# Optimization experiments

Hardware: AMD Instinct MI355X
Metric: run time of the kernel (lower is better)

Reference implementation:

```python
import jax, jax.numpy as jnp
import numpy as np

PAD = 1
K = 3  # kernel_size


def conv2d(x, w, b):
    y = jax.lax.conv_general_dilated(
        x, w, window_strides=(1, 1), padding=((PAD, PAD), (PAD, PAD)),
        dimension_numbers=("NCHW", "OIHW", "NCHW"))
    return y + b[None, :, None, None]


def deform_conv2d(x, offset, weight, bias):
    # torchvision.ops.deform_conv2d semantics (stride=1, dilation=1, 1 offset group)
    B, C, H, W = x.shape
    O = weight.shape[0]
    K2 = K * K
    off = offset.reshape(B, K2, 2, H, W)  # [...,0]=dy, [...,1]=dx
    ky, kx = jnp.meshgrid(jnp.arange(K), jnp.arange(K), indexing="ij")
    ky = ky.reshape(K2).astype(x.dtype)
    kx = kx.reshape(K2).astype(x.dtype)
    hh = jnp.arange(H, dtype=x.dtype)
    ww = jnp.arange(W, dtype=x.dtype)
    # sampling coords, shape [B, K2, H, W]
    py = off[:, :, 0] + ky[None, :, None, None] + hh[None, None, :, None] - PAD
    px = off[:, :, 1] + kx[None, :, None, None] + ww[None, None, None, :] - PAD

    y0 = jnp.floor(py)
    x0 = jnp.floor(px)
    wy = (py - y0)[:, None]  # [B,1,K2,H,W]
    wx = (px - x0)[:, None]

    xf = x.reshape(B, C, H * W)

    def gather(iy, ix):
        valid = (iy >= 0) & (iy < H) & (ix >= 0) & (ix < W)
        iyc = jnp.clip(iy, 0, H - 1).astype(jnp.int32)
        ixc = jnp.clip(ix, 0, W - 1).astype(jnp.int32)
        idx = (iyc * W + ixc).reshape(B, 1, K2 * H * W)
        v = jnp.take_along_axis(xf, idx, axis=2).reshape(B, C, K2, H, W)
        return v * valid.reshape(B, 1, K2, H, W).astype(x.dtype)

    v00 = gather(y0, x0)
    v01 = gather(y0, x0 + 1)
    v10 = gather(y0 + 1, x0)
    v11 = gather(y0 + 1, x0 + 1)
    sampled = (v00 * (1 - wy) * (1 - wx) + v01 * (1 - wy) * wx
               + v10 * wy * (1 - wx) + v11 * wy * wx)  # [B,C,K2,H,W]
    out = jnp.einsum("bckhw,ock->bohw", sampled, weight.reshape(O, C, K2))
    return out + bias[None, :, None, None]


def setup_inputs() -> dict:
    key = jax.random.key(0)
    k1, k2, k3, k4, k5 = jax.random.split(key, 5)
    B, C, H, W = 4, 64, 192, 192
    O = 64
    x = jax.random.normal(k1, (B, C, H, W), dtype=jnp.float32)
    w_off = jax.random.normal(k2, (2 * K * K, C, K, K), dtype=jnp.float32) * 0.05
    b_off = jnp.zeros((2 * K * K,), dtype=jnp.float32)
    w_conv = jax.random.normal(k3, (O, C, K, K), dtype=jnp.float32) * (1.0 / np.sqrt(C * K * K))
    b_conv = jax.random.normal(k4, (O,), dtype=jnp.float32) * 0.01
    return {"x": x, "w_off": w_off, "b_off": b_off, "w_conv": w_conv, "b_conv": b_conv}


def reference(x, w_off, b_off, w_conv, b_conv):
    offset = conv2d(x, w_off, b_off)
    y = deform_conv2d(x, offset, w_conv, b_conv)
    return conv2d(y, w_conv, b_conv)  # module reuses self.conv on deform output
```

## Files before the change

kernel.cpp:

```cpp
#include <hip/hip_runtime.h>

constexpr int B = 4;
constexpr int C = 64;
constexpr int O = 64;
constexpr int OOFF = 18;
constexpr int H = 192;
constexpr int W = 192;

typedef __attribute__((ext_vector_type(8))) short short8;
typedef __attribute__((ext_vector_type(4))) float float4v;

__device__ inline ushort f2bf(float f) {
  unsigned u = __float_as_uint(f);
  unsigned r = (u + 0x7fffu + ((u >> 16) & 1u)) >> 16;
  return (ushort)r;
}

__global__ __launch_bounds__(256) void k_prep_wB(const float* __restrict__ w_conv,
                                                 ushort* __restrict__ wBf) {
  const int i = blockIdx.x * 256 + threadIdx.x;
  if (i >= 9 * 2 * 4 * 64 * 8) return;
  const int j = i & 7;
  const int lane = (i >> 3) & 63;
  const int nt = (i >> 9) & 3;
  const int kstep = (i >> 11) & 1;
  const int kk = i >> 12;
  const int n = nt + 4 * (lane & 15);
  const int c = kstep * 32 + ((lane >> 4) & 3) * 8 + j;
  wBf[i] = f2bf(w_conv[((size_t)n * C + c) * 9 + kk]);
}

__global__ __launch_bounds__(256) void k_prep_wOff(const float* __restrict__ w_off,
                                                   ushort* __restrict__ wOf) {
  const int i = blockIdx.x * 256 + threadIdx.x;
  if (i >= 9 * 2 * 2 * 64 * 8) return;
  const int j = i & 7;
  const int lane = (i >> 3) & 63;
  const int nt = (i >> 9) & 1;
  const int ks = (i >> 10) & 1;
  const int kk = i >> 11;
  const int n = nt * 16 + (lane & 15);
  const int c = ks * 32 + ((lane >> 4) & 3) * 8 + j;
  wOf[i] = (n < OOFF) ? f2bf(w_off[((size_t)n * C + c) * 9 + kk]) : (ushort)0;
}

__global__ __launch_bounds__(256) void k_transpose_bf(const float* __restrict__ x,
                                                      ushort* __restrict__ xtb) {
  __shared__ float tile[64][17];
  const int w0 = blockIdx.x * 16;
  const int h = blockIdx.y;
  const int b = blockIdx.z;
  const int tid = threadIdx.x;

  const int wl = tid & 15;
  const int c0 = tid >> 4;
#pragma unroll
  for (int r = 0; r < 4; ++r) {
    const int c = c0 + r * 16;
    tile[c][wl] = x[(((size_t)b * C + c) * H + h) * W + w0 + wl];
  }
  __syncthreads();
  const int c = tid & 63;
  const int qq = tid >> 6;
#pragma unroll
  for (int r = 0; r < 4; ++r) {
    const int wq = qq + r * 4;
    xtb[(((size_t)b * H + h) * W + w0 + wq) * C + c] = f2bf(tile[c][wq]);
  }
}

__global__ __launch_bounds__(256) void k_conv_off_mfma(
    const ushort* __restrict__ xtb, const ushort* __restrict__ wOf,
    const float* __restrict__ b_off, float* __restrict__ offp) {
  const int w0 = blockIdx.x * 16;
  const int b = blockIdx.z;
  const int tid = threadIdx.x;
  const int wave = tid >> 6, lane = tid & 63;
  const int col = lane & 15, quad = lane >> 4;
  const int h0 = blockIdx.y * 8 + wave * 2;

  float4v acc[2][2];
#pragma unroll
  for (int mt = 0; mt < 2; ++mt)
#pragma unroll
    for (int nt = 0; nt < 2; ++nt) acc[mt][nt] = (float4v){0.f, 0.f, 0.f, 0.f};

#pragma unroll 1
  for (int kk = 0; kk < 9; ++kk) {
    const int ky = kk / 3, kx = kk % 3;
    const int ww = w0 + col + kx - 1;
    const bool wok = (unsigned)ww < (unsigned)W;
    const int wwc = min(max(ww, 0), W - 1);

    short8 bfr[2][2];
#pragma unroll
    for (int ks = 0; ks < 2; ++ks)
#pragma unroll
      for (int nt = 0; nt < 2; ++nt)
        bfr[ks][nt] = *(const short8*)&wOf[((((size_t)kk * 2 + ks) * 2 + nt) * 64 + lane) * 8];

    short8 afr[2][2];
#pragma unroll
    for (int mt = 0; mt < 2; ++mt) {
      const int hh = h0 + mt + ky - 1;
      const bool ok = wok && ((unsigned)hh < (unsigned)H);
      const int hhc = min(max(hh, 0), H - 1);
      const ushort* pa = xtb + (((size_t)b * H + hhc) * W + wwc) * C + quad * 8;
#pragma unroll
      for (int ks = 0; ks < 2; ++ks) {
        short8 v = (short8)0;
        if (ok) v = *(const short8*)(pa + ks * 32);
        afr[mt][ks] = v;
      }
    }
#pragma unroll
    for (int ks = 0; ks < 2; ++ks)
#pragma unroll
      for (int mt = 0; mt < 2; ++mt)
#pragma unroll
        for (int nt = 0; nt < 2; ++nt)
          acc[mt][nt] = __builtin_amdgcn_mfma_f32_16x16x32_bf16(afr[mt][ks], bfr[ks][nt],
                                                                acc[mt][nt], 0, 0, 0);
  }

#pragma unroll
  for (int mt = 0; mt < 2; ++mt) {
    const int h = h0 + mt;
#pragma unroll
    for (int nt = 0; nt < 2; ++nt) {
      const int o = nt * 16 + col;
      if (o < OOFF) {
        const float bias = b_off[o];
#pragma unroll
        for (int r = 0; r < 4; ++r) {
          const int w = w0 + quad * 4 + r;
          offp[(((size_t)b * H + h) * W + w) * OOFF + o] = acc[mt][nt][r] + bias;
        }
      }
    }
  }
}

__global__ __launch_bounds__(256, 3) void k_deform_mfma(
    const ushort* __restrict__ xtb, const float* __restrict__ offp,
    const ushort* __restrict__ wBf, const float* __restrict__ b_conv,
    ushort* __restrict__ yt) {
  __shared__ ushort sA[2][2][4][64][8];

  const int bid = blockIdx.x;
  const int xcd = bid & 7;
  const int s = bid >> 3;
  const int b = xcd >> 1;
  const int half = xcd & 1;
  const int th = half * 12 + s / 24;
  const int tw = s % 24;
  const int h0 = th * 8, w0 = tw * 8;

  const int tid = threadIdx.x;
  const int wave = tid >> 6, lane = tid & 63;
  const int p = tid >> 2, qtr = tid & 3;
  const int prow = p >> 3, pcol = p & 7;
  const int h = h0 + prow, w = w0 + pcol;
  const int ks_w = qtr >> 1;
  const int q2 = (qtr & 1) * 2;

  const float* po = offp + ((size_t)(b * H + h) * W + w) * OOFF;
  float2 offv[9];
#pragma unroll
  for (int kk = 0; kk < 9; ++kk) offv[kk] = *(const float2*)(po + 2 * kk);

  const ushort* xb = xtb + (size_t)b * H * W * C + qtr * 16;

  uint4 G[2][8];
  float4 aw[2];

  auto issue = [&](int kk, int buf) {
    const float dy = offv[kk].x, dx = offv[kk].y;
    const int ky = kk / 3, kx = kk % 3;
    const float pyf = dy + (float)(ky + h - 1);
    const float pxf = dx + (float)(kx + w - 1);
    const float fy0 = floorf(pyf), fx0 = floorf(pxf);
    const float wy = pyf - fy0, wx = pxf - fx0;
    const int iy0 = (int)fy0, ix0 = (int)fx0;
    const int iy1 = iy0 + 1, ix1 = ix0 + 1;
    const bool vy0 = (unsigned)iy0 < (unsigned)H;
    const bool vy1 = (unsigned)iy1 < (unsigned)H;
    const bool vx0 = (unsigned)ix0 < (unsigned)W;
    const bool vx1 = (unsigned)ix1 < (unsigned)W;
    aw[buf].x = (vy0 && vx0) ? (1.f - wy) * (1.f - wx) : 0.f;
    aw[buf].y = (vy0 && vx1) ? (1.f - wy) * wx : 0.f;
    aw[buf].z = (vy1 && vx0) ? wy * (1.f - wx) : 0.f;
    aw[buf].w = (vy1 && vx1) ? wy * wx : 0.f;
    const int cy0 = min(max(iy0, 0), H - 1), cy1 = min(max(iy1, 0), H - 1);
    const int cx0 = min(max(ix0, 0), W - 1), cx1 = min(max(ix1, 0), W - 1);
    const uint4* p00 = (const uint4*)(xb + ((size_t)cy0 * W + cx0) * C);
    const uint4* p01 = (const uint4*)(xb + ((size_t)cy0 * W + cx1) * C);
    const uint4* p10 = (const uint4*)(xb + ((size_t)cy1 * W + cx0) * C);
    const uint4* p11 = (const uint4*)(xb + ((size_t)cy1 * W + cx1) * C);
    G[buf][0] = p00[0]; G[buf][1] = p00[1];
    G[buf][2] = p01[0]; G[buf][3] = p01[1];
    G[buf][4] = p10[0]; G[buf][5] = p10[1];
    G[buf][6] = p11[0]; G[buf][7] = p11[1];
  };

  float4v acc[4];
#pragma unroll
  for (int nt = 0; nt < 4; ++nt) acc[nt] = (float4v){0.f, 0.f, 0.f, 0.f};

  issue(0, 0);
#pragma unroll
  for (int kk = 0; kk < 9; ++kk) {
    const int buf = kk & 1;
    if (kk < 8) issue(kk + 1, buf ^ 1);

    const float a00 = aw[buf].x, a01 = aw[buf].y;
    const float a10 = aw[buf].z, a11 = aw[buf].w;
    uint pk[8];
#pragma unroll
    for (int i = 0; i < 8; ++i) {
      const uint u00 = ((const uint*)&G[buf][0])[i];
      const uint u01 = ((const uint*)&G[buf][2])[i];
      const uint u10 = ((const uint*)&G[buf][4])[i];
      const uint u11 = ((const uint*)&G[buf][6])[i];
      const float lo = __uint_as_float(u00 << 16) * a00 + __uint_as_float(u01 << 16) * a01 +
                       __uint_as_float(u10 << 16) * a10 + __uint_as_float(u11 << 16) * a11;
      const float hi = __uint_as_float(u00 & 0xffff0000u) * a00 +
                       __uint_as_float(u01 & 0xffff0000u) * a01 +
                       __uint_as_float(u10 & 0xffff0000u) * a10 +
                       __uint_as_float(u11 & 0xffff0000u) * a11;
      pk[i] = (uint)f2bf(lo) | ((uint)f2bf(hi) << 16);
    }
    *(uint4*)&sA[buf][ks_w][p >> 4][(p & 15) | (q2 << 4)][0] = *(const uint4*)&pk[0];
    *(uint4*)&sA[buf][ks_w][p >> 4][(p & 15) | ((q2 + 1) << 4)][0] = *(const uint4*)&pk[4];
    __syncthreads();

#pragma unroll
    for (int ks = 0; ks < 2; ++ks) {
      const short8 a = *(const short8*)&sA[buf][ks][wave][lane][0];
#pragma unroll
      for (int nt = 0; nt < 4; ++nt) {
        const short8 bb = *(const short8*)&wBf[((((size_t)kk * 2 + ks) * 4 + nt) * 64 + lane) * 8];
        acc[nt] = __builtin_amdgcn_mfma_f32_16x16x32_bf16(a, bb, acc[nt], 0, 0, 0);
      }
    }
  }

  const int quad = lane >> 4, c16 = lane & 15;
  float bias[4];
#pragma unroll
  for (int nt = 0; nt < 4; ++nt) bias[nt] = b_conv[4 * c16 + nt];
#pragma unroll
  for (int r = 0; r < 4; ++r) {
    const int pp = wave * 16 + quad * 4 + r;
    const int hrow = h0 + (pp >> 3), wcol = w0 + (pp & 7);
    uint2 u;
    u.x = (uint)f2bf(acc[0][r] + bias[0]) | ((uint)f2bf(acc[1][r] + bias[1]) << 16);
    u.y = (uint)f2bf(acc[2][r] + bias[2]) | ((uint)f2bf(acc[3][r] + bias[3]) << 16);
    *(uint2*)&yt[((size_t)(b * H + hrow) * W + wcol) * C + 4 * c16] = u;
  }
}

__global__ __launch_bounds__(256) void k_conv_main_mfma(
    const ushort* __restrict__ yt, const ushort* __restrict__ wBf,
    const float* __restrict__ b_conv, float* __restrict__ out) {
  const int w0 = blockIdx.x * 16;
  const int b = blockIdx.z;
  const int tid = threadIdx.x;
  const int wave = tid >> 6, lane = tid & 63;
  const int col = lane & 15, quad = lane >> 4;
  const int h0 = blockIdx.y * 8 + wave * 2;

  float4v acc[2][4];
#pragma unroll
  for (int mt = 0; mt < 2; ++mt)
#pragma unroll
    for (int nt = 0; nt < 4; ++nt) acc[mt][nt] = (float4v){0.f, 0.f, 0.f, 0.f};

#pragma unroll 1
  for (int kk = 0; kk < 9; ++kk) {
    const int ky = kk / 3, kx = kk % 3;
    const int ww = w0 + col + kx - 1;
    const bool wok = (unsigned)ww < (unsigned)W;
    const int wwc = min(max(ww, 0), W - 1);

    short8 bfr[2][4];
#pragma unroll
    for (int ks = 0; ks < 2; ++ks)
#pragma unroll
      for (int nt = 0; nt < 4; ++nt)
        bfr[ks][nt] = *(const short8*)&wBf[((((size_t)kk * 2 + ks) * 4 + nt) * 64 + lane) * 8];

    short8 afr[2][2];
#pragma unroll
    for (int mt = 0; mt < 2; ++mt) {
      const int hh = h0 + mt + ky - 1;
      const bool ok = wok && ((unsigned)hh < (unsigned)H);
      const int hhc = min(max(hh, 0), H - 1);
      const ushort* pa = yt + (((size_t)b * H + hhc) * W + wwc) * C + quad * 8;
#pragma unroll
      for (int ks = 0; ks < 2; ++ks) {
        short8 v = (short8)0;
        if (ok) v = *(const short8*)(pa + ks * 32);
        afr[mt][ks] = v;
      }
    }
#pragma unroll
    for (int ks = 0; ks < 2; ++ks)
#pragma unroll
      for (int mt = 0; mt < 2; ++mt)
#pragma unroll
        for (int nt = 0; nt < 4; ++nt)
          acc[mt][nt] = __builtin_amdgcn_mfma_f32_16x16x32_bf16(afr[mt][ks], bfr[ks][nt],
                                                                acc[mt][nt], 0, 0, 0);
  }

  float bias[4];
#pragma unroll
  for (int nt = 0; nt < 4; ++nt) bias[nt] = b_conv[4 * col + nt];
#pragma unroll
  for (int mt = 0; mt < 2; ++mt) {
    const int h = h0 + mt;
#pragma unroll
    for (int nt = 0; nt < 4; ++nt) {
      const int oc = 4 * col + nt;
      float4 v;
      v.x = acc[mt][nt][0] + bias[nt];
      v.y = acc[mt][nt][1] + bias[nt];
      v.z = acc[mt][nt][2] + bias[nt];
      v.w = acc[mt][nt][3] + bias[nt];
      *(float4*)&out[(((size_t)b * O + oc) * H + h) * W + w0 + quad * 4] = v;
    }
  }
}

extern "C" void kernel_launch(void* const* d_in, const int* in_sizes, int n_in,
                              void* d_out, int out_size, void* d_ws, size_t ws_size,
                              hipStream_t stream) {
  const float* x = (const float*)d_in[0];
  const float* w_off = (const float*)d_in[1];
  const float* b_off = (const float*)d_in[2];
  const float* w_conv = (const float*)d_in[3];
  const float* b_conv = (const float*)d_in[4];
  float* out = (float*)d_out;

  float* offp = (float*)d_ws;
  ushort* xtb = (ushort*)(offp + (size_t)B * H * W * OOFF);
  ushort* yt = xtb + (size_t)B * H * W * C;
  ushort* wBf = yt + (size_t)B * H * W * C;
  ushort* wOf = wBf + 36864;

  const dim3 blk(256);
  k_prep_wB<<<dim3(144), blk, 0, stream>>>(w_conv, wBf);
  k_prep_wOff<<<dim3(72), blk, 0, stream>>>(w_off, wOf);
  k_transpose_bf<<<dim3(W / 16, H, B), blk, 0, stream>>>(x, xtb);
  k_conv_off_mfma<<<dim3(W / 16, H / 8, B), blk, 0, stream>>>(xtb, wOf, b_off, offp);
  k_deform_mfma<<<dim3(2304), blk, 0, stream>>>(xtb, offp, wBf, b_conv, yt);
  k_conv_main_mfma<<<dim3(W / 16, H / 8, B), blk, 0, stream>>>(yt, wBf, b_conv, out);
}
```

Before: 224.0 us.

## Merge prep kernels, software-pipeline conv loads, use packed bf16 conversions

Folds the two weight-prep kernels and the x transpose into a single launch, removing two kernel launches. Both MFMA convolution kernels now fully unroll the 9-tap loop and double-buffer the A/B fragment loads so the next tap's global loads overlap the current tap's MFMAs. The deform bilinear blend uses packed 2-wide float math, and bf16 rounding now goes through native __bf16 conversions, which may map to hardware pack instructions. The extra prefetch buffers raise register pressure and may lower occupancy.

```diff
diff --git a/kernel.cpp b/kernel.cpp
--- a/kernel.cpp
+++ b/kernel.cpp
@@ -9,63 +9,74 @@
 
 typedef __attribute__((ext_vector_type(8))) short short8;
 typedef __attribute__((ext_vector_type(4))) float float4v;
+typedef __attribute__((ext_vector_type(2))) float f32x2;
+typedef __attribute__((ext_vector_type(2))) uint u32x2;
+typedef __attribute__((ext_vector_type(2))) __bf16 bf16x2;
 
 __device__ inline ushort f2bf(float f) {
-  unsigned u = __float_as_uint(f);
-  unsigned r = (u + 0x7fffu + ((u >> 16) & 1u)) >> 16;
-  return (ushort)r;
-}
-
-__global__ __launch_bounds__(256) void k_prep_wB(const float* __restrict__ w_conv,
-                                                 ushort* __restrict__ wBf) {
-  const int i = blockIdx.x * 256 + threadIdx.x;
-  if (i >= 9 * 2 * 4 * 64 * 8) return;
-  const int j = i & 7;
-  const int lane = (i >> 3) & 63;
-  const int nt = (i >> 9) & 3;
-  const int kstep = (i >> 11) & 1;
-  const int kk = i >> 12;
-  const int n = nt + 4 * (lane & 15);
-  const int c = kstep * 32 + ((lane >> 4) & 3) * 8 + j;
-  wBf[i] = f2bf(w_conv[((size_t)n * C + c) * 9 + kk]);
-}
-
-__global__ __launch_bounds__(256) void k_prep_wOff(const float* __restrict__ w_off,
-                                                   ushort* __restrict__ wOf) {
-  const int i = blockIdx.x * 256 + threadIdx.x;
-  if (i >= 9 * 2 * 2 * 64 * 8) return;
-  const int j = i & 7;
-  const int lane = (i >> 3) & 63;
-  const int nt = (i >> 9) & 1;
-  const int ks = (i >> 10) & 1;
-  const int kk = i >> 11;
-  const int n = nt * 16 + (lane & 15);
-  const int c = ks * 32 + ((lane >> 4) & 3) * 8 + j;
-  wOf[i] = (n < OOFF) ? f2bf(w_off[((size_t)n * C + c) * 9 + kk]) : (ushort)0;
-}
-
-__global__ __launch_bounds__(256) void k_transpose_bf(const float* __restrict__ x,
-                                                      ushort* __restrict__ xtb) {
+  return __builtin_bit_cast(ushort, (__bf16)f);
+}
+__device__ inline uint pk2bf(float lo, float hi) {
+  bf16x2 v;
+  v.x = (__bf16)lo;
+  v.y = (__bf16)hi;
+  return __builtin_bit_cast(uint, v);
+}
+__device__ inline f32x2 upk(uint u) {
+  u32x2 t;
+  t.x = u << 16;
+  t.y = u & 0xffff0000u;
+  return __builtin_bit_cast(f32x2, t);
+}
+
+__global__ __launch_bounds__(256) void k_pre(const float* __restrict__ x,
+                                             ushort* __restrict__ xtb,
+                                             const float* __restrict__ w_conv,
+                                             ushort* __restrict__ wBf,
+                                             const float* __restrict__ w_off,
+                                             ushort* __restrict__ wOf) {
   __shared__ float tile[64][17];
-  const int w0 = blockIdx.x * 16;
-  const int h = blockIdx.y;
-  const int b = blockIdx.z;
+  const int bid = blockIdx.x;
   const int tid = threadIdx.x;
-
-  const int wl = tid & 15;
-  const int c0 = tid >> 4;
-#pragma unroll
-  for (int r = 0; r < 4; ++r) {
-    const int c = c0 + r * 16;
-    tile[c][wl] = x[(((size_t)b * C + c) * H + h) * W + w0 + wl];
-  }
-  __syncthreads();
-  const int c = tid & 63;
-  const int qq = tid >> 6;
-#pragma unroll
-  for (int r = 0; r < 4; ++r) {
-    const int wq = qq + r * 4;
-    xtb[(((size_t)b * H + h) * W + w0 + wq) * C + c] = f2bf(tile[c][wq]);
+  if (bid < 9216) {
+    const int w0 = (bid % 12) * 16;
+    const int h = (bid / 12) % 192;
+    const int b = bid / 2304;
+    const int wl = tid & 15;
+    const int c0 = tid >> 4;
+#pragma unroll
+    for (int r = 0; r < 4; ++r) {
+      const int c = c0 + r * 16;
+      tile[c][wl] = x[(((size_t)b * C + c) * H + h) * W + w0 + wl];
+    }
+    __syncthreads();
+    const int c = tid & 63;
+    const int qq = tid >> 6;
+#pragma unroll
+    for (int r = 0; r < 4; ++r) {
+      const int wq = qq + r * 4;
+      xtb[(((size_t)b * H + h) * W + w0 + wq) * C + c] = f2bf(tile[c][wq]);
+    }
+  } else if (bid < 9360) {
+    const int i = (bid - 9216) * 256 + tid;
+    const int j = i & 7;
+    const int lane = (i >> 3) & 63;
+    const int nt = (i >> 9) & 3;
+    const int kstep = (i >> 11) & 1;
+    const int kk = i >> 12;
+    const int n = nt + 4 * (lane & 15);
+    const int c = kstep * 32 + ((lane >> 4) & 3) * 8 + j;
+    wBf[i] = f2bf(w_conv[((size_t)n * C + c) * 9 + kk]);
+  } else {
+    const int i = (bid - 9360) * 256 + tid;
+    const int j = i & 7;
+    const int lane = (i >> 3) & 63;
+    const int nt = (i >> 9) & 1;
+    const int ks = (i >> 10) & 1;
+    const int kk = i >> 11;
+    const int n = nt * 16 + (lane & 15);
+    const int c = ks * 32 + ((lane >> 4) & 3) * 8 + j;
+    wOf[i] = (n < OOFF) ? f2bf(w_off[((size_t)n * C + c) * 9 + kk]) : (ushort)0;
   }
 }
 
@@ -85,21 +96,19 @@
 #pragma unroll
     for (int nt = 0; nt < 2; ++nt) acc[mt][nt] = (float4v){0.f, 0.f, 0.f, 0.f};
 
-#pragma unroll 1
-  for (int kk = 0; kk < 9; ++kk) {
+  short8 bfr[2][2][2];
+  short8 afr[2][2][2];
+
+  auto load = [&](int kk, int pb) {
     const int ky = kk / 3, kx = kk % 3;
     const int ww = w0 + col + kx - 1;
     const bool wok = (unsigned)ww < (unsigned)W;
     const int wwc = min(max(ww, 0), W - 1);
-
-    short8 bfr[2][2];
 #pragma unroll
     for (int ks = 0; ks < 2; ++ks)
 #pragma unroll
       for (int nt = 0; nt < 2; ++nt)
-        bfr[ks][nt] = *(const short8*)&wOf[((((size_t)kk * 2 + ks) * 2 + nt) * 64 + lane) * 8];
-
-    short8 afr[2][2];
+        bfr[pb][ks][nt] = *(const short8*)&wOf[((((size_t)kk * 2 + ks) * 2 + nt) * 64 + lane) * 8];
 #pragma unroll
     for (int mt = 0; mt < 2; ++mt) {
       const int hh = h0 + mt + ky - 1;
@@ -110,16 +119,23 @@
       for (int ks = 0; ks < 2; ++ks) {
         short8 v = (short8)0;
         if (ok) v = *(const short8*)(pa + ks * 32);
-        afr[mt][ks] = v;
+        afr[pb][mt][ks] = v;
       }
     }
+  };
+
+  load(0, 0);
+#pragma unroll
+  for (int kk = 0; kk < 9; ++kk) {
+    const int pb = kk & 1;
+    if (kk < 8) load(kk + 1, pb ^ 1);
 #pragma unroll
     for (int ks = 0; ks < 2; ++ks)
 #pragma unroll
       for (int mt = 0; mt < 2; ++mt)
 #pragma unroll
         for (int nt = 0; nt < 2; ++nt)
-          acc[mt][nt] = __builtin_amdgcn_mfma_f32_16x16x32_bf16(afr[mt][ks], bfr[ks][nt],
+          acc[mt][nt] = __builtin_amdgcn_mfma_f32_16x16x32_bf16(afr[pb][mt][ks], bfr[pb][ks][nt],
                                                                 acc[mt][nt], 0, 0, 0);
   }
 
@@ -213,8 +229,10 @@
     const int buf = kk & 1;
     if (kk < 8) issue(kk + 1, buf ^ 1);
 
-    const float a00 = aw[buf].x, a01 = aw[buf].y;
-    const float a10 = aw[buf].z, a11 = aw[buf].w;
+    const f32x2 a00 = {aw[buf].x, aw[buf].x};
+    const f32x2 a01 = {aw[buf].y, aw[buf].y};
+    const f32x2 a10 = {aw[buf].z, aw[buf].z};
+    const f32x2 a11 = {aw[buf].w, aw[buf].w};
     uint pk[8];
 #pragma unroll
     for (int i = 0; i < 8; ++i) {
@@ -222,13 +240,8 @@
       const uint u01 = ((const uint*)&G[buf][2])[i];
       const uint u10 = ((const uint*)&G[buf][4])[i];
       const uint u11 = ((const uint*)&G[buf][6])[i];
-      const float lo = __uint_as_float(u00 << 16) * a00 + __uint_as_float(u01 << 16) * a01 +
-                       __uint_as_float(u10 << 16) * a10 + __uint_as_float(u11 << 16) * a11;
-      const float hi = __uint_as_float(u00 & 0xffff0000u) * a00 +
-                       __uint_as_float(u01 & 0xffff0000u) * a01 +
-                       __uint_as_float(u10 & 0xffff0000u) * a10 +
-                       __uint_as_float(u11 & 0xffff0000u) * a11;
-      pk[i] = (uint)f2bf(lo) | ((uint)f2bf(hi) << 16);
+      f32x2 sv = upk(u00) * a00 + upk(u01) * a01 + upk(u10) * a10 + upk(u11) * a11;
+      pk[i] = pk2bf(sv.x, sv.y);
     }
     *(uint4*)&sA[buf][ks_w][p >> 4][(p & 15) | (q2 << 4)][0] = *(const uint4*)&pk[0];
     *(uint4*)&sA[buf][ks_w][p >> 4][(p & 15) | ((q2 + 1) << 4)][0] = *(const uint4*)&pk[4];
@@ -254,8 +267,8 @@
     const int pp = wave * 16 + quad * 4 + r;
     const int hrow = h0 + (pp >> 3), wcol = w0 + (pp & 7);
     uint2 u;
-    u.x = (uint)f2bf(acc[0][r] + bias[0]) | ((uint)f2bf(acc[1][r] + bias[1]) << 16);
-    u.y = (uint)f2bf(acc[2][r] + bias[2]) | ((uint)f2bf(acc[3][r] + bias[3]) << 16);
+    u.x = pk2bf(acc[0][r] + bias[0], acc[1][r] + bias[1]);
+    u.y = pk2bf(acc[2][r] + bias[2], acc[3][r] + bias[3]);
     *(uint2*)&yt[((size_t)(b * H + hrow) * W + wcol) * C + 4 * c16] = u;
   }
 }
@@ -276,21 +289,19 @@
 #pragma unroll
     for (int nt = 0; nt < 4; ++nt) acc[mt][nt] = (float4v){0.f, 0.f, 0.f, 0.f};
 
-#pragma unroll 1
-  for (int kk = 0; kk < 9; ++kk) {
+  short8 bfr[2][2][4];
+  short8 afr[2][2][2];
+
+  auto load = [&](int kk, int pb) {
     const int ky = kk / 3, kx = kk % 3;
     const int ww = w0 + col + kx - 1;
     const bool wok = (unsigned)ww < (unsigned)W;
     const int wwc = min(max(ww, 0), W - 1);
-
-    short8 bfr[2][4];
 #pragma unroll
     for (int ks = 0; ks < 2; ++ks)
 #pragma unroll
       for (int nt = 0; nt < 4; ++nt)
-        bfr[ks][nt] = *(const short8*)&wBf[((((size_t)kk * 2 + ks) * 4 + nt) * 64 + lane) * 8];
-
-    short8 afr[2][2];
+        bfr[pb][ks][nt] = *(const short8*)&wBf[((((size_t)kk * 2 + ks) * 4 + nt) * 64 + lane) * 8];
 #pragma unroll
     for (int mt = 0; mt < 2; ++mt) {
       const int hh = h0 + mt + ky - 1;
@@ -301,16 +312,23 @@
       for (int ks = 0; ks < 2; ++ks) {
         short8 v = (short8)0;
         if (ok) v = *(const short8*)(pa + ks * 32);
-        afr[mt][ks] = v;
+        afr[pb][mt][ks] = v;
       }
     }
+  };
+
+  load(0, 0);
+#pragma unroll
+  for (int kk = 0; kk < 9; ++kk) {
+    const int pb = kk & 1;
+    if (kk < 8) load(kk + 1, pb ^ 1);
 #pragma unroll
     for (int ks = 0; ks < 2; ++ks)
 #pragma unroll
       for (int mt = 0; mt < 2; ++mt)
 #pragma unroll
         for (int nt = 0; nt < 4; ++nt)
-          acc[mt][nt] = __builtin_amdgcn_mfma_f32_16x16x32_bf16(afr[mt][ks], bfr[ks][nt],
+          acc[mt][nt] = __builtin_amdgcn_mfma_f32_16x16x32_bf16(afr[pb][mt][ks], bfr[pb][ks][nt],
                                                                 acc[mt][nt], 0, 0, 0);
   }
 
@@ -350,9 +368,7 @@
   ushort* wOf = wBf + 36864;
 
   const dim3 blk(256);
-  k_prep_wB<<<dim3(144), blk, 0, stream>>>(w_conv, wBf);
-  k_prep_wOff<<<dim3(72), blk, 0, stream>>>(w_off, wOf);
-  k_transpose_bf<<<dim3(W / 16, H, B), blk, 0, stream>>>(x, xtb);
+  k_pre<<<dim3(9432), blk, 0, stream>>>(x, xtb, w_conv, wBf, w_off, wOf);
   k_conv_off_mfma<<<dim3(W / 16, H / 8, B), blk, 0, stream>>>(xtb, wOf, b_off, offp);
   k_deform_mfma<<<dim3(2304), blk, 0, stream>>>(xtb, offp, wBf, b_conv, yt);
   k_conv_main_mfma<<<dim3(W / 16, H / 8, B), blk, 0, stream>>>(yt, wBf, b_conv, out);
```

New measurement: 209.8 us. 6.3% less time.
